# Optimization experiments

Measured on AMD Instinct MI355X. Metric: run time of the kernel, lower is better.

Reference implementation:

```python
import jax, jax.numpy as jnp
import numpy as np

T = 0.2


def _cdist(a, b):
    # Euclidean cdist with zero-safe sqrt (grad 0 at coincident points, like torch)
    d2 = (a * a).sum(-1)[:, None] + (b * b).sum(-1)[None, :] - 2.0 * (a @ b.T)
    d2 = jnp.maximum(d2, 0.0)
    safe = jnp.where(d2 > 0, d2, 1.0)
    return jnp.where(d2 > 0, jnp.sqrt(safe), 0.0)


def _generator(eps, W_in, b_in, W_blk, b_blk, W_out, b_out):
    x = eps @ W_in.T + b_in
    for i in range(W_blk.shape[0]):  # 4 residual MLP blocks
        x = x + jax.nn.relu(x @ W_blk[i].T + b_blk[i])
    return x @ W_out.T + b_out


def setup_inputs() -> dict:
    N, D, H = 4096, 128, 512
    key = jax.random.key(0)
    ks = jax.random.split(key, 16)

    def lin(kw, kb, fan_in, shape_w, shape_b):
        bound = 1.0 / np.sqrt(fan_in)
        W = jax.random.uniform(kw, shape_w, jnp.float32, -bound, bound)
        b = jax.random.uniform(kb, shape_b, jnp.float32, -bound, bound)
        return W, b

    W_in, b_in = lin(ks[0], ks[1], D, (H, D), (H,))
    W_blk, b_blk = lin(ks[2], ks[3], H, (4, H, H), (4, H))
    W_out, b_out = lin(ks[4], ks[5], H, (D, H), (D,))
    y_pos = jax.random.normal(ks[6], (N, D), jnp.float32)
    eps = jax.random.normal(ks[7], (N, D), jnp.float32)
    return {"y_pos": y_pos, "eps": eps, "W_in": W_in, "b_in": b_in,
            "W_blk": W_blk, "b_blk": b_blk, "W_out": W_out, "b_out": b_out}


def reference(y_pos, eps, W_in, b_in, W_blk, b_blk, W_out, b_out):
    x = _generator(eps, W_in, b_in, W_blk, b_blk, W_out, b_out)  # [N, D]
    N = y_pos.shape[0]
    dist_pos = _cdist(x, y_pos)                                   # [N, N]
    dist_neg = _cdist(x, x) + jnp.eye(x.shape[0], dtype=x.dtype) * 1e6
    A = jnp.concatenate([-dist_pos / T, -dist_neg / T], axis=-1)  # [N, 2N]
    A_row = jax.nn.softmax(A, axis=-1)
    A_col = jax.nn.softmax(A, axis=-2)
    A_soft = jnp.sqrt(A_row * A_col)
    A_pos = A_soft[:, :N]
    A_neg = A_soft[:, N:]
    s_pos = A_pos.sum(axis=1, keepdims=True)
    s_neg = A_neg.sum(axis=1, keepdims=True)
    Wpos = A_pos * s_neg
    # torch in-place: Wpos *= s_neg mutates A_pos BEFORE A_pos.sum is taken,
    # so Wneg = A_neg * (A_pos * s_neg).sum(1) = A_neg * s_pos * s_neg
    Wneg = A_neg * (s_pos * s_neg)
    V = Wpos @ y_pos - Wneg @ x                                   # drifting field
    target = jax.lax.stop_gradient(x + V)
    return jnp.mean((x - target) ** 2)
```

## Files before the change

kernel.cpp:

```cpp
#include <hip/hip_runtime.h>
#include <math.h>

#define N 4096
#define D 128
#define H 512
#define KSPLIT 4
#define SC_LOG2 7.2134752044f

typedef short bf16x8 __attribute__((ext_vector_type(8)));
typedef float f32x4 __attribute__((ext_vector_type(4)));
typedef unsigned short u16x8 __attribute__((ext_vector_type(8)));
typedef unsigned short u16;
typedef _Float16 f16;
typedef _Float16 f16x4 __attribute__((ext_vector_type(4)));

#define MFMA(a, b, c) __builtin_amdgcn_mfma_f32_16x16x32_bf16((a), (b), (c), 0, 0, 0)
#define SCHED_FENCE() __builtin_amdgcn_sched_barrier(0)

__device__ __forceinline__ float fexp2(float x)
{
#if __has_builtin(__builtin_amdgcn_exp2f)
    return __builtin_amdgcn_exp2f(x);
#else
    return exp2f(x);
#endif
}

__device__ __forceinline__ float fsqrt(float x)
{
#if __has_builtin(__builtin_amdgcn_sqrtf)
    return __builtin_amdgcn_sqrtf(x);
#else
    return sqrtf(x);
#endif
}

__device__ __forceinline__ float bf2f(u16 h)
{
    return __uint_as_float(((unsigned)h) << 16);
}

__device__ __forceinline__ u16 rtn_bf16(float v)
{
    unsigned u = __float_as_uint(v);
    return (u16)((u + 0x7FFFu + ((u >> 16) & 1u)) >> 16);
}

__device__ __forceinline__ void split1(float v, u16& h, u16& l)
{
    u16 hh = rtn_bf16(v);
    float r = v - bf2f(hh);
    h = hh;
    l = rtn_bf16(r);
}

__device__ __forceinline__ void split1_trunc(float v, u16& h, u16& l)
{
    unsigned bv = __float_as_uint(v);
    unsigned hb = bv & 0xFFFF0000u;
    float r = v - __uint_as_float(hb);
    h = (u16)(hb >> 16);
    l = (u16)(__float_as_uint(r) >> 16);
}

template <int CTRL>
__device__ __forceinline__ float dppf(float x)
{
    int r = __builtin_amdgcn_update_dpp(0, __float_as_int(x), CTRL, 0xF, 0xF, true);
    return __int_as_float(r);
}

struct SplitDesc { const float* src; u16* h; int n; };
struct SplitArgs { SplitDesc d[4]; };

__global__ __launch_bounds__(256) void split_multi(SplitArgs args)
{
    SplitDesc de = args.d[blockIdx.y];
    int idx = (blockIdx.x * 256 + threadIdx.x) * 4;
    if (idx >= de.n) return;
    float4 v = *(const float4*)(de.src + idx);
    ushort4 hv;
    hv.x = rtn_bf16(v.x); hv.y = rtn_bf16(v.y);
    hv.z = rtn_bf16(v.z); hv.w = rtn_bf16(v.w);
    *(ushort4*)(de.h + idx) = hv;
}

template <int K, bool RR>
__device__ __forceinline__ void gen_layer(
    u16 (&XhS)[16][520], u16 (&XlS)[16][520],
    const u16* __restrict__ W, const float* __restrict__ bias,
    int w, int quad, int l16)
{
    const int nb = w * 64;
    constexpr int NT = K >> 5;
    constexpr int PF = NT < 4 ? NT : 4;
    f32x4 acc[4] = {};
    const u16* wp[4];
    #pragma unroll
    for (int ni = 0; ni < 4; ++ni)
        wp[ni] = W + (size_t)(nb + ni * 16 + l16) * K + quad * 8;
    float bl4[4];
    #pragma unroll
    for (int ni = 0; ni < 4; ++ni) bl4[ni] = bias[nb + ni * 16 + l16];
    bf16x8 B[PF][4];
    #pragma unroll
    for (int s = 0; s < PF; ++s)
        #pragma unroll
        for (int ni = 0; ni < 4; ++ni)
            B[s][ni] = *(const bf16x8*)(wp[ni] + s * 32);
    SCHED_FENCE();
    #pragma unroll
    for (int kt = 0; kt < NT; ++kt) {
        const int kk = kt * 32 + quad * 8;
        bf16x8 af  = *(const bf16x8*)&XhS[l16][kk];
        bf16x8 alf = *(const bf16x8*)&XlS[l16][kk];
        #pragma unroll
        for (int ni = 0; ni < 4; ++ni) {
            acc[ni] = MFMA(af,  B[kt % PF][ni], acc[ni]);
            acc[ni] = MFMA(alf, B[kt % PF][ni], acc[ni]);
        }
        SCHED_FENCE();
        if (kt + PF < NT) {
            #pragma unroll
            for (int ni = 0; ni < 4; ++ni)
                B[kt % PF][ni] = *(const bf16x8*)(wp[ni] + (kt + PF) * 32);
        }
        SCHED_FENCE();
    }
    __syncthreads();
    #pragma unroll
    for (int ni = 0; ni < 4; ++ni) {
        const int col = nb + ni * 16 + l16;
        #pragma unroll
        for (int r = 0; r < 4; ++r) {
            const int row = quad * 4 + r;
            float v = acc[ni][r] + bl4[ni];
            if (RR) {
                float prev = bf2f(XhS[row][col]) + bf2f(XlS[row][col]);
                v = prev + fmaxf(v, 0.0f);
            }
            u16 hh, ll;
            split1_trunc(v, hh, ll);
            XhS[row][col] = hh;
            XlS[row][col] = ll;
        }
    }
    __syncthreads();
}

__global__ __launch_bounds__(512, 2) void gen_fused(
    const float* __restrict__ eps,
    const u16* __restrict__ Win, const u16* __restrict__ Wblk,
    const u16* __restrict__ Wout,
    const float* __restrict__ b_in, const float* __restrict__ b_blk,
    const float* __restrict__ b_out,
    float* __restrict__ xo, u16* __restrict__ xh)
{
    __shared__ u16 XhS[16][520], XlS[16][520];
    const int t = threadIdx.x;
    const int w = t >> 6, lane = t & 63;
    const int quad = lane >> 4, l16 = lane & 15;
    const int bm = blockIdx.x * 16;

    {
        int idx = t * 4;
        int row = idx >> 7, col = idx & 127;
        float4 v = *(const float4*)(eps + (size_t)(bm + row) * D + col);
        ushort4 hv, lv;
        split1(v.x, hv.x, lv.x); split1(v.y, hv.y, lv.y);
        split1(v.z, hv.z, lv.z); split1(v.w, hv.w, lv.w);
        *(ushort4*)&XhS[row][col] = hv;
        *(ushort4*)&XlS[row][col] = lv;
    }
    __syncthreads();

    gen_layer<D, false>(XhS, XlS, Win, b_in, w, quad, l16);
    for (int i = 0; i < 4; ++i)
        gen_layer<H, true>(XhS, XlS, Wblk + (size_t)i * H * H, b_blk + i * H,
                           w, quad, l16);

    {
        const int n0 = w * 16;
        constexpr int NT = H >> 5;
        constexpr int PF = 4;
        f32x4 acc5 = {};
        const u16* wp = Wout + (size_t)(n0 + l16) * H + quad * 8;
        const float bl = b_out[n0 + l16];
        bf16x8 B5[PF];
        #pragma unroll
        for (int s = 0; s < PF; ++s)
            B5[s] = *(const bf16x8*)(wp + s * 32);
        SCHED_FENCE();
        #pragma unroll
        for (int kt = 0; kt < NT; ++kt) {
            const int kk = kt * 32 + quad * 8;
            bf16x8 af  = *(const bf16x8*)&XhS[l16][kk];
            bf16x8 alf = *(const bf16x8*)&XlS[l16][kk];
            acc5 = MFMA(af,  B5[kt % PF], acc5);
            acc5 = MFMA(alf, B5[kt % PF], acc5);
            SCHED_FENCE();
            if (kt + PF < NT)
                B5[kt % PF] = *(const bf16x8*)(wp + (kt + PF) * 32);
            SCHED_FENCE();
        }
        const int col = n0 + l16;
        #pragma unroll
        for (int r = 0; r < 4; ++r) {
            const int gm = bm + quad * 4 + r;
            float v = acc5[r] + bl;
            xo[(size_t)gm * D + col] = v;
            xh[(size_t)gm * D + col] = rtn_bf16(v);
        }
    }
}

__global__ __launch_bounds__(256) void rownorm(
    const float* __restrict__ X, const float* __restrict__ Y,
    float* __restrict__ nx, float* __restrict__ ny)
{
    const float* src = blockIdx.y ? Y : X;
    float* dst = blockIdx.y ? ny : nx;
    const int t = threadIdx.x;
    const int row = blockIdx.x * 64 + (t >> 2);
    const int q = t & 3;
    const float* rp = src + (size_t)row * D + q * 32;
    float s = 0.f;
    #pragma unroll
    for (int i = 0; i < 8; ++i) {
        float4 v = *(const float4*)(rp + i * 4);
        s += v.x * v.x + v.y * v.y + v.z * v.z + v.w * v.w;
    }
    s += __shfl_xor(s, 1);
    s += __shfl_xor(s, 2);
    if (q == 0) dst[row] = s;
}

__global__ __launch_bounds__(256) void transpose_rtn(
    const float* __restrict__ X, const float* __restrict__ Y,
    u16* __restrict__ Xth, u16* __restrict__ Yth)
{
    const float* src = blockIdx.z ? Y : X;
    u16* th = blockIdx.z ? Yth : Xth;
    __shared__ float tile[32][33];
    const int t = threadIdx.x;
    const int r0 = blockIdx.x * 32, c0 = blockIdx.y * 32;
    {
        int rit = t >> 3, coff = (t & 7) * 4;
        float4 v = *(const float4*)(src + (size_t)(r0 + rit) * D + c0 + coff);
        tile[rit][coff + 0] = v.x; tile[rit][coff + 1] = v.y;
        tile[rit][coff + 2] = v.z; tile[rit][coff + 3] = v.w;
    }
    __syncthreads();
    {
        int cit = t >> 3, roff = (t & 7) * 4;
        ushort4 hv;
        hv.x = rtn_bf16(tile[roff + 0][cit]);
        hv.y = rtn_bf16(tile[roff + 1][cit]);
        hv.z = rtn_bf16(tile[roff + 2][cit]);
        hv.w = rtn_bf16(tile[roff + 3][cit]);
        *(ushort4*)(th + (size_t)(c0 + cit) * N + r0 + roff) = hv;
    }
}

__global__ __launch_bounds__(256) void dist_fused(
    const u16* __restrict__ Xh, const u16* __restrict__ Yh,
    const float* __restrict__ nx, const float* __restrict__ ny,
    f16* __restrict__ Apos, f16* __restrict__ Aneg,
    float* __restrict__ prm_p, float* __restrict__ prs_p,
    float* __restrict__ pcm_p, float* __restrict__ pcs_p,
    float* __restrict__ prm_n, float* __restrict__ prs_n)
{
    const int mat = blockIdx.z;
    const u16* Bhp = mat ? Xh : Yh;
    const float* nb = mat ? nx : ny;
    f16* Out = mat ? Aneg : Apos;
    float* prm = mat ? prm_n : prm_p;
    float* prs = mat ? prs_n : prs_p;

    __shared__ u16 XhS[128][40], YhS[128][40];
    const int t = threadIdx.x;
    const int w = t >> 6, lane = t & 63;
    const int quad = lane >> 4, l16 = lane & 15;
    const int bm = blockIdx.y * 128, bn = blockIdx.x * 128;
    f32x4 acc[2][8] = {};

    for (int k0 = 0; k0 < D; k0 += 32) {
        __syncthreads();
        #pragma unroll
        for (int p = 0; p < 2; ++p) {
            int slot = t + p * 256;
            int row = slot >> 2, koff = (slot & 3) << 3;
            *(u16x8*)&XhS[row][koff] =
                *(const u16x8*)(Xh + (size_t)(bm + row) * D + k0 + koff);
        }
        #pragma unroll
        for (int p = 0; p < 2; ++p) {
            int slot = t + p * 256;
            int row = slot >> 2, koff = (slot & 3) << 3;
            int pr = ((row & 3) << 4) | ((row & 63) >> 2) | (row & 64);
            int kf = koff ^ (((pr >> 4) & 3) << 3);
            *(u16x8*)&YhS[pr][kf] =
                *(const u16x8*)(Bhp + (size_t)(bn + row) * D + k0 + koff);
        }
        __syncthreads();
        bf16x8 af[2], bhf[8];
        #pragma unroll
        for (int mi = 0; mi < 2; ++mi)
            af[mi] = *(const bf16x8*)&XhS[w * 32 + mi * 16 + l16][quad * 8];
        #pragma unroll
        for (int ni = 0; ni < 8; ++ni) {
            int nn = ni & 3, hf = ni >> 2;
            bhf[ni] = *(const bf16x8*)
                &YhS[hf * 64 + nn * 16 + l16][(quad * 8) ^ (nn << 3)];
        }
        #pragma unroll
        for (int mi = 0; mi < 2; ++mi)
            #pragma unroll
            for (int ni = 0; ni < 8; ++ni)
                acc[mi][ni] = MFMA(af[mi], bhf[ni], acc[mi][ni]);
    }
    const int jb = bn + (l16 << 2);
    const float SC2 = SC_LOG2 * SC_LOG2;
    const float c2 = -2.0f * SC2;
    const float4 n0v = *(const float4*)(nb + jb);
    const float4 n1v = *(const float4*)(nb + jb + 64);
    const float nl[8] = {n0v.x * SC2, n0v.y * SC2, n0v.z * SC2, n0v.w * SC2,
                         n1v.x * SC2, n1v.y * SC2, n1v.z * SC2, n1v.w * SC2};
    #pragma unroll
    for (int mi = 0; mi < 2; ++mi)
        #pragma unroll
        for (int r = 0; r < 4; ++r) {
            const int gm = bm + w * 32 + mi * 16 + quad * 4 + r;
            const float nxm = nx[gm] * SC2;
            f16x4 ov0, ov1;
            #pragma unroll
            for (int nn = 0; nn < 4; ++nn) {
                float s0 = fsqrt(fmaxf(
                    fmaf(acc[mi][nn][r], c2, nxm + nl[nn]), 0.f));
                float s1 = fsqrt(fmaxf(
                    fmaf(acc[mi][4 + nn][r], c2, nxm + nl[4 + nn]), 0.f));
                if (mat) {
                    if (gm == jb + nn) s0 = 5.0e6f;
                    if (gm == jb + 64 + nn) s1 = 5.0e6f;
                }
                acc[mi][nn][r] = s0;
                acc[mi][4 + nn][r] = s1;
                ov0[nn] = (f16)(-s0);
                ov1[nn] = (f16)(-s1);
            }
            *(f16x4*)(Out + (size_t)gm * N + jb) = ov0;
            *(f16x4*)(Out + (size_t)gm * N + jb + 64) = ov1;
        }
    float m[2][4];
    #pragma unroll
    for (int mi = 0; mi < 2; ++mi)
        #pragma unroll
        for (int r = 0; r < 4; ++r) {
            float v = fminf(fminf(fminf(acc[mi][0][r], acc[mi][1][r]),
                                  fminf(acc[mi][2][r], acc[mi][3][r])),
                            fminf(fminf(acc[mi][4][r], acc[mi][5][r]),
                                  fminf(acc[mi][6][r], acc[mi][7][r])));
            v = fminf(v, dppf<0xB1>(v));
            v = fminf(v, dppf<0x4E>(v));
            v = fminf(v, dppf<0x141>(v));
            v = fminf(v, dppf<0x140>(v));
            m[mi][r] = v;
        }
    float mn = fminf(fminf(fminf(m[0][0], m[0][1]), fminf(m[0][2], m[0][3])),
                     fminf(fminf(m[1][0], m[1][1]), fminf(m[1][2], m[1][3])));
    mn = fminf(mn, __shfl_xor(mn, 16));
    mn = fminf(mn, __shfl_xor(mn, 32));
    float sig[2][4] = {};
    float cs[8] = {};
    #pragma unroll
    for (int mi = 0; mi < 2; ++mi)
        #pragma unroll
        for (int ni = 0; ni < 8; ++ni) {
            float e0 = fexp2(mn - acc[mi][ni][0]);
            float e1 = fexp2(mn - acc[mi][ni][1]);
            float e2 = fexp2(mn - acc[mi][ni][2]);
            float e3 = fexp2(mn - acc[mi][ni][3]);
            sig[mi][0] += e0; sig[mi][1] += e1;
            sig[mi][2] += e2; sig[mi][3] += e3;
            cs[ni] += (e0 + e1) + (e2 + e3);
        }
    const int ct = blockIdx.x;
    #pragma unroll
    for (int mi = 0; mi < 2; ++mi)
        #pragma unroll
        for (int r = 0; r < 4; ++r) {
            float s = sig[mi][r];
            s += dppf<0xB1>(s);
            s += dppf<0x4E>(s);
            s += dppf<0x141>(s);
            s += dppf<0x140>(s);
            s *= fexp2(m[mi][r] - mn);
            if (l16 == 0) {
                int grow = bm + w * 32 + mi * 16 + quad * 4 + r;
                prm[(size_t)ct * N + grow] = -m[mi][r];
                prs[(size_t)ct * N + grow] = s;
            }
        }
    if (mat == 0) {
        const int rt = blockIdx.y * 4 + w;
        #pragma unroll
        for (int ni = 0; ni < 8; ++ni) {
            cs[ni] += __shfl_xor(cs[ni], 16);
            cs[ni] += __shfl_xor(cs[ni], 32);
        }
        if (quad == 0) {
            float4 c0 = {cs[0], cs[1], cs[2], cs[3]};
            float4 c1 = {cs[4], cs[5], cs[6], cs[7]};
            float4 m4 = {-mn, -mn, -mn, -mn};
            *(float4*)(pcs_p + (size_t)rt * N + jb) = c0;
            *(float4*)(pcs_p + (size_t)rt * N + jb + 64) = c1;
            *(float4*)(pcm_p + (size_t)rt * N + jb) = m4;
            *(float4*)(pcm_p + (size_t)rt * N + jb + 64) = m4;
        }
    }
}

__global__ __launch_bounds__(256) void stats_combine(
    const float* __restrict__ prm_p, const float* __restrict__ prs_p,
    const float* __restrict__ prm_n, const float* __restrict__ prs_n,
    const float* __restrict__ pcm_p, const float* __restrict__ pcs_p,
    float* __restrict__ m_row, float* __restrict__ isr,
    float* __restrict__ m_col, float* __restrict__ isc)
{
    __shared__ float Ms[4][64], Ss[4][64];
    const int t = threadIdx.x;
    const int g = t >> 6, l = t & 63;
    const int idx = blockIdx.x * 64 + l;

    float m = -3.0e38f, s = 0.f;
    if (idx < N) {
        const int i = idx;
        const int c0 = g * 8;
        #pragma unroll 4
        for (int c = c0; c < c0 + 8; ++c) {
            m = fmaxf(m, prm_p[(size_t)c * N + i]);
            m = fmaxf(m, prm_n[(size_t)c * N + i]);
        }
        #pragma unroll 4
        for (int c = c0; c < c0 + 8; ++c) {
            s += prs_p[(size_t)c * N + i] * fexp2(prm_p[(size_t)c * N + i] - m);
            s += prs_n[(size_t)c * N + i] * fexp2(prm_n[(size_t)c * N + i] - m);
        }
    } else {
        const int mat = (idx - N) >> 12;
        const int j = idx & (N - 1);
        const float* pm = mat ? prm_n : pcm_p;
        const float* ps = mat ? prs_n : pcs_p;
        const int cnt = mat ? 8 : 32;
        const int cb = g * cnt;
        #pragma unroll 4
        for (int c = cb; c < cb + cnt; ++c)
            m = fmaxf(m, pm[(size_t)c * N + j]);
        #pragma unroll 4
        for (int c = cb; c < cb + cnt; ++c)
            s += ps[(size_t)c * N + j] * fexp2(pm[(size_t)c * N + j] - m);
    }
    Ms[g][l] = m; Ss[g][l] = s;
    __syncthreads();
    if (g == 0) {
        float m0 = Ms[0][l], m1 = Ms[1][l], m2 = Ms[2][l], m3 = Ms[3][l];
        float mm = fmaxf(fmaxf(m0, m1), fmaxf(m2, m3));
        float ss = Ss[0][l] * fexp2(m0 - mm) + Ss[1][l] * fexp2(m1 - mm)
                 + Ss[2][l] * fexp2(m2 - mm) + Ss[3][l] * fexp2(m3 - mm);
        if (idx < N) {
            m_row[idx] = mm;
            isr[idx] = 1.0f / sqrtf(ss);
        } else {
            const int mat = (idx - N) >> 12;
            const int j = idx & (N - 1);
            m_col[mat * N + j] = mm;
            isc[mat * N + j] = 1.0f / sqrtf(ss);
        }
    }
}

__global__ __launch_bounds__(256) void pv_mfma(
    const f16* __restrict__ Apos, const f16* __restrict__ Aneg,
    const u16* __restrict__ Yth, const u16* __restrict__ Xth,
    const float* __restrict__ m_row, const float* __restrict__ isr,
    const float* __restrict__ m_col, const float* __restrict__ isc,
    float* __restrict__ u_part, float* __restrict__ w_part,
    float* __restrict__ sp_part, float* __restrict__ sn_part)
{
    const int mat = blockIdx.z;
    const f16* Am = mat ? Aneg : Apos;
    const u16* Bh = mat ? Xth : Yth;
    const float* mc = m_col + mat * N;
    const float* ic = isc + mat * N;
    float* Cp = (mat ? w_part : u_part) + (size_t)blockIdx.y * (N * D);
    float* spn = (mat ? sn_part : sp_part) + (size_t)blockIdx.y * N;

    __shared__ u16 BhS[128][72];
    __shared__ u16 PhS[64][72], PlS[64][72];
    __shared__ float mrS[64], isrS[64];

    const int t = threadIdx.x;
    const int w = t >> 6, lane = t & 63;
    const int quad = lane >> 4, l16 = lane & 15;
    const int bm = blockIdx.x * 64;
    const int jbase = blockIdx.y * (N / KSPLIT);
    const int arow = t >> 4;
    const int aj = (t & 15) << 2;

    if (t < 64) { mrS[t] = m_row[bm + t]; isrS[t] = isr[bm + t]; }

    f32x4 acc[8] = {};
    float rs[4] = {0.f, 0.f, 0.f, 0.f};

    for (int jt = 0; jt < (N / KSPLIT) / 64; ++jt) {
        const int j0 = jbase + jt * 64;
        __syncthreads();
        #pragma unroll
        for (int p = 0; p < 4; ++p) {
            int slot = t + p * 256;
            int d = slot >> 3, joff = (slot & 7) << 3;
            *(u16x8*)&BhS[d][joff] = *(const u16x8*)(Bh + (size_t)d * N + j0 + joff);
        }
        float4 mcv = *(const float4*)(mc + j0 + aj);
        float4 icv = *(const float4*)(ic + j0 + aj);
        #pragma unroll
        for (int s = 0; s < 4; ++s) {
            int row = arow + s * 16;
            f16x4 av = *(const f16x4*)(Am + (size_t)(bm + row) * N + j0 + aj);
            float mr = mrS[row], sr = isrS[row];
            float p0 = fexp2((float)av.x - 0.5f * (mr + mcv.x)) * (sr * icv.x);
            float p1 = fexp2((float)av.y - 0.5f * (mr + mcv.y)) * (sr * icv.y);
            float p2 = fexp2((float)av.z - 0.5f * (mr + mcv.z)) * (sr * icv.z);
            float p3 = fexp2((float)av.w - 0.5f * (mr + mcv.w)) * (sr * icv.w);
            rs[s] += p0 + p1 + p2 + p3;
            ushort4 hv, lv;
            split1_trunc(p0, hv.x, lv.x); split1_trunc(p1, hv.y, lv.y);
            split1_trunc(p2, hv.z, lv.z); split1_trunc(p3, hv.w, lv.w);
            *(ushort4*)&PhS[row][aj] = hv;
            *(ushort4*)&PlS[row][aj] = lv;
        }
        __syncthreads();
        #pragma unroll
        for (int ks = 0; ks < 2; ++ks) {
            const int kk = ks * 32 + quad * 8;
            bf16x8 ph = *(const bf16x8*)&PhS[w * 16 + l16][kk];
            bf16x8 pl = *(const bf16x8*)&PlS[w * 16 + l16][kk];
            #pragma unroll
            for (int ni = 0; ni < 8; ++ni) {
                bf16x8 bh = *(const bf16x8*)&BhS[ni * 16 + l16][kk];
                acc[ni] = MFMA(ph, bh, acc[ni]);
                acc[ni] = MFMA(pl, bh, acc[ni]);
            }
        }
    }
    #pragma unroll
    for (int ni = 0; ni < 8; ++ni)
        #pragma unroll
        for (int r = 0; r < 4; ++r) {
            int row = w * 16 + quad * 4 + r;
            int col = ni * 16 + l16;
            Cp[(size_t)(bm + row) * D + col] = acc[ni][r];
        }
    #pragma unroll
    for (int s = 0; s < 4; ++s) {
        float v = rs[s];
        v += __shfl_xor(v, 1); v += __shfl_xor(v, 2);
        v += __shfl_xor(v, 4); v += __shfl_xor(v, 8);
        if (l16 == 0) spn[bm + arow + s * 16] = v;
    }
}

__global__ __launch_bounds__(256) void final_reduce(const float* __restrict__ u_part,
    const float* __restrict__ w_part, const float* __restrict__ sp_part,
    const float* __restrict__ sn_part, double* __restrict__ acc_part)
{
    __shared__ float red[256];
    const int t = threadIdx.x;
    const int idx = blockIdx.x * 256 + t;
    float u = 0.f, w = 0.f;
    #pragma unroll
    for (int c = 0; c < KSPLIT; ++c) {
        u += u_part[(size_t)c * (N * D) + idx];
        w += w_part[(size_t)c * (N * D) + idx];
    }
    const int i = idx >> 7;
    float sp = 0.f, sn = 0.f;
    #pragma unroll
    for (int c = 0; c < KSPLIT; ++c) {
        sp += sp_part[(size_t)c * N + i];
        sn += sn_part[(size_t)c * N + i];
    }
    const float v = sn * u - sp * sn * w;
    red[t] = v * v; __syncthreads();
    for (int s = 128; s > 0; s >>= 1) { if (t < s) red[t] += red[t + s]; __syncthreads(); }
    if (!t) acc_part[blockIdx.x] = (double)red[0];
}

__global__ __launch_bounds__(256) void finalize(const double* __restrict__ acc_part,
                                                float* __restrict__ out)
{
    __shared__ double red[256];
    const int t = threadIdx.x;
    double s = 0.0;
    #pragma unroll
    for (int i = 0; i < 8; ++i) s += acc_part[t + i * 256];
    red[t] = s; __syncthreads();
    for (int st = 128; st > 0; st >>= 1) {
        if (t < st) red[t] += red[t + st];
        __syncthreads();
    }
    if (!t) out[0] = (float)(red[0] * (1.0 / ((double)N * (double)D)));
}

extern "C" void kernel_launch(void* const* d_in, const int* in_sizes, int n_in,
                              void* d_out, int out_size, void* d_ws, size_t ws_size,
                              hipStream_t stream)
{
    const float* y_pos = (const float*)d_in[0];
    const float* eps   = (const float*)d_in[1];
    const float* W_in  = (const float*)d_in[2];
    const float* b_in  = (const float*)d_in[3];
    const float* W_blk = (const float*)d_in[4];
    const float* b_blk = (const float*)d_in[5];
    const float* W_out = (const float*)d_in[6];
    const float* b_out = (const float*)d_in[7];
    float* out = (float*)d_out;
    (void)in_sizes; (void)n_in; (void)out_size; (void)ws_size;

    char* p = (char*)d_ws;
    auto alloc = [&](size_t bytes) {
        char* r = p;
        p += (bytes + 255) & ~(size_t)255;
        return r;
    };
    double* acc_part = (double*)alloc(2048 * 8);
    float* sp_part = (float*)alloc((size_t)KSPLIT * N * 4);
    float* sn_part = (float*)alloc((size_t)KSPLIT * N * 4);
    float* m_row  = (float*)alloc(N * 4);
    float* isr    = (float*)alloc(N * 4);
    float* m_col  = (float*)alloc(2 * N * 4);
    float* isc    = (float*)alloc(2 * N * 4);
    float* nx     = (float*)alloc(N * 4);
    float* ny     = (float*)alloc(N * 4);
    float* xo  = (float*)alloc((size_t)N * D * 4);
    u16* xh    = (u16*)alloc((size_t)N * D * 2);
    u16* xth   = (u16*)alloc((size_t)N * D * 2);
    u16* yh    = (u16*)alloc((size_t)N * D * 2);
    u16* yth   = (u16*)alloc((size_t)N * D * 2);
    char* genreg = alloc((size_t)KSPLIT * N * D * 4 * 2);
    u16* wih = (u16*)genreg;
    u16* wbh = wih + (size_t)H * D;
    u16* woh = wbh + (size_t)4 * H * H;
    float* prm_p = (float*)genreg;
    float* prs_p = prm_p + 32 * N;
    float* prm_n = prs_p + 32 * N;
    float* prs_n = prm_n + 32 * N;
    float* pcm_p = prs_n + 32 * N;
    float* pcs_p = pcm_p + 128 * N;
    float* u_part = (float*)genreg;
    float* w_part = u_part + (size_t)KSPLIT * N * D;
    f16* Apos = (f16*)alloc((size_t)N * N * 2);
    f16* Aneg = (f16*)alloc((size_t)N * N * 2);

    SplitArgs sa;
    sa.d[0] = { y_pos, yh,  N * D };
    sa.d[1] = { W_in,  wih, H * D };
    sa.d[2] = { W_blk, wbh, 4 * H * H };
    sa.d[3] = { W_out, woh, D * H };
    split_multi<<<dim3(1024, 4), 256, 0, stream>>>(sa);

    gen_fused<<<N / 16, 512, 0, stream>>>(eps, wih, wbh, woh,
                                          b_in, b_blk, b_out, xo, xh);

    rownorm<<<dim3(N / 64, 2), 256, 0, stream>>>(xo, y_pos, nx, ny);

    transpose_rtn<<<dim3(N / 32, D / 32, 2), 256, 0, stream>>>(
        xo, y_pos, xth, yth);

    dist_fused<<<dim3(N / 128, N / 128, 2), 256, 0, stream>>>(
        xh, yh, nx, ny, Apos, Aneg,
        prm_p, prs_p, pcm_p, pcs_p, prm_n, prs_n);

    stats_combine<<<192, 256, 0, stream>>>(prm_p, prs_p, prm_n, prs_n,
                                           pcm_p, pcs_p,
                                           m_row, isr, m_col, isc);

    pv_mfma<<<dim3(N / 64, KSPLIT, 2), 256, 0, stream>>>(Apos, Aneg,
        yth, xth, m_row, isr, m_col, isc, u_part, w_part, sp_part, sn_part);

    final_reduce<<<(N * D) / 256, 256, 0, stream>>>(u_part, w_part,
                                                    sp_part, sn_part, acc_part);
    finalize<<<1, 256, 0, stream>>>(acc_part, out);
}
```

Baseline: 230.3 us.

## Pre-pack generator weights into MFMA fragment layout and use 1024-thread blocks

The weight conversion kernel now writes generator weights in a packed layout ordered by k-tile, quad and output column, so each lane's bf16x8 fragment load is contiguous across the wavefront and coalesced. The fused generator kernel moves to 1024 threads with 16 waves, each owning 32 output columns instead of 64. The explicit register prefetch pipeline and scheduling fences are dropped in favour of a simple two-k-tile unrolled loop. This halves per-wave accumulators and register pressure and improves weight-load coalescing, but it relies on the compiler to hide global load latency and leaves half the waves idle in the output layer.

```diff
diff --git a/kernel.cpp b/kernel.cpp
--- a/kernel.cpp
+++ b/kernel.cpp
@@ -15,7 +15,6 @@
 typedef _Float16 f16x4 __attribute__((ext_vector_type(4)));
 
 #define MFMA(a, b, c) __builtin_amdgcn_mfma_f32_16x16x32_bf16((a), (b), (c), 0, 0, 0)
-#define SCHED_FENCE() __builtin_amdgcn_sched_barrier(0)
 
 __device__ __forceinline__ float fexp2(float x)
 {
@@ -70,7 +69,7 @@
     return __int_as_float(r);
 }
 
-struct SplitDesc { const float* src; u16* h; int n; };
+struct SplitDesc { const float* src; u16* h; int n; int ks; int os; };
 struct SplitArgs { SplitDesc d[4]; };
 
 __global__ __launch_bounds__(256) void split_multi(SplitArgs args)
@@ -82,59 +81,63 @@
     ushort4 hv;
     hv.x = rtn_bf16(v.x); hv.y = rtn_bf16(v.y);
     hv.z = rtn_bf16(v.z); hv.w = rtn_bf16(v.w);
-    *(ushort4*)(de.h + idx) = hv;
+    if (de.ks < 0) {
+        *(ushort4*)(de.h + idx) = hv;
+    } else {
+        const int ks = de.ks, os = de.os;
+        const int lsz = 1 << (ks + os);
+        const int layer = idx >> (ks + os);
+        const int fl = idx & (lsz - 1);
+        const int col = fl >> ks;
+        const int k = fl & ((1 << ks) - 1);
+        const int kt = k >> 5, quad = (k >> 3) & 3, j = k & 7;
+        const int pidx = layer * lsz + (((((kt << 2) + quad) << os) + col) << 3) + j;
+        *(ushort4*)(de.h + pidx) = hv;
+    }
 }
 
 template <int K, bool RR>
 __device__ __forceinline__ void gen_layer(
     u16 (&XhS)[16][520], u16 (&XlS)[16][520],
-    const u16* __restrict__ W, const float* __restrict__ bias,
+    const u16* __restrict__ Wp, const float* __restrict__ bias,
     int w, int quad, int l16)
 {
-    const int nb = w * 64;
+    const int nb = w * 32;
     constexpr int NT = K >> 5;
-    constexpr int PF = NT < 4 ? NT : 4;
-    f32x4 acc[4] = {};
-    const u16* wp[4];
-    #pragma unroll
-    for (int ni = 0; ni < 4; ++ni)
-        wp[ni] = W + (size_t)(nb + ni * 16 + l16) * K + quad * 8;
-    float bl4[4];
-    #pragma unroll
-    for (int ni = 0; ni < 4; ++ni) bl4[ni] = bias[nb + ni * 16 + l16];
-    bf16x8 B[PF][4];
-    #pragma unroll
-    for (int s = 0; s < PF; ++s)
-        #pragma unroll
-        for (int ni = 0; ni < 4; ++ni)
-            B[s][ni] = *(const bf16x8*)(wp[ni] + s * 32);
-    SCHED_FENCE();
-    #pragma unroll
-    for (int kt = 0; kt < NT; ++kt) {
-        const int kk = kt * 32 + quad * 8;
-        bf16x8 af  = *(const bf16x8*)&XhS[l16][kk];
-        bf16x8 alf = *(const bf16x8*)&XlS[l16][kk];
-        #pragma unroll
-        for (int ni = 0; ni < 4; ++ni) {
-            acc[ni] = MFMA(af,  B[kt % PF][ni], acc[ni]);
-            acc[ni] = MFMA(alf, B[kt % PF][ni], acc[ni]);
-        }
-        SCHED_FENCE();
-        if (kt + PF < NT) {
-            #pragma unroll
-            for (int ni = 0; ni < 4; ++ni)
-                B[kt % PF][ni] = *(const bf16x8*)(wp[ni] + (kt + PF) * 32);
-        }
-        SCHED_FENCE();
+    f32x4 acc[2] = {};
+    float bl2[2];
+    bl2[0] = bias[nb + l16];
+    bl2[1] = bias[nb + 16 + l16];
+    const u16* wb = Wp + (size_t)quad * 4096 + (size_t)nb * 8 + (size_t)l16 * 8;
+    #pragma unroll
+    for (int kc = 0; kc < NT / 2; ++kc) {
+        const int kta = 2 * kc, ktb = 2 * kc + 1;
+        bf16x8 b0[2], b1[2];
+        b0[0] = *(const bf16x8*)(wb + kta * 16384);
+        b0[1] = *(const bf16x8*)(wb + kta * 16384 + 128);
+        b1[0] = *(const bf16x8*)(wb + ktb * 16384);
+        b1[1] = *(const bf16x8*)(wb + ktb * 16384 + 128);
+        bf16x8 a0h = *(const bf16x8*)&XhS[l16][kta * 32 + quad * 8];
+        bf16x8 a0l = *(const bf16x8*)&XlS[l16][kta * 32 + quad * 8];
+        bf16x8 a1h = *(const bf16x8*)&XhS[l16][ktb * 32 + quad * 8];
+        bf16x8 a1l = *(const bf16x8*)&XlS[l16][ktb * 32 + quad * 8];
+        acc[0] = MFMA(a0h, b0[0], acc[0]);
+        acc[0] = MFMA(a0l, b0[0], acc[0]);
+        acc[1] = MFMA(a0h, b0[1], acc[1]);
+        acc[1] = MFMA(a0l, b0[1], acc[1]);
+        acc[0] = MFMA(a1h, b1[0], acc[0]);
+        acc[0] = MFMA(a1l, b1[0], acc[0]);
+        acc[1] = MFMA(a1h, b1[1], acc[1]);
+        acc[1] = MFMA(a1l, b1[1], acc[1]);
     }
     __syncthreads();
     #pragma unroll
-    for (int ni = 0; ni < 4; ++ni) {
+    for (int ni = 0; ni < 2; ++ni) {
         const int col = nb + ni * 16 + l16;
         #pragma unroll
         for (int r = 0; r < 4; ++r) {
             const int row = quad * 4 + r;
-            float v = acc[ni][r] + bl4[ni];
+            float v = acc[ni][r] + bl2[ni];
             if (RR) {
                 float prev = bf2f(XhS[row][col]) + bf2f(XlS[row][col]);
                 v = prev + fmaxf(v, 0.0f);
@@ -148,7 +151,7 @@
     __syncthreads();
 }
 
-__global__ __launch_bounds__(512, 2) void gen_fused(
+__global__ __launch_bounds__(1024) void gen_fused(
     const float* __restrict__ eps,
     const u16* __restrict__ Win, const u16* __restrict__ Wblk,
     const u16* __restrict__ Wout,
@@ -163,45 +166,42 @@
     const int bm = blockIdx.x * 16;
 
     {
-        int idx = t * 4;
+        int idx = t * 2;
         int row = idx >> 7, col = idx & 127;
-        float4 v = *(const float4*)(eps + (size_t)(bm + row) * D + col);
-        ushort4 hv, lv;
+        float2 v = *(const float2*)(eps + (size_t)(bm + row) * D + col);
+        ushort2 hv, lv;
         split1(v.x, hv.x, lv.x); split1(v.y, hv.y, lv.y);
-        split1(v.z, hv.z, lv.z); split1(v.w, hv.w, lv.w);
-        *(ushort4*)&XhS[row][col] = hv;
-        *(ushort4*)&XlS[row][col] = lv;
+        *(ushort2*)&XhS[row][col] = hv;
+        *(ushort2*)&XlS[row][col] = lv;
     }
     __syncthreads();
 
     gen_layer<D, false>(XhS, XlS, Win, b_in, w, quad, l16);
+    #pragma unroll 1
     for (int i = 0; i < 4; ++i)
         gen_layer<H, true>(XhS, XlS, Wblk + (size_t)i * H * H, b_blk + i * H,
                            w, quad, l16);
 
-    {
+    if (w < 8) {
         const int n0 = w * 16;
         constexpr int NT = H >> 5;
-        constexpr int PF = 4;
         f32x4 acc5 = {};
-        const u16* wp = Wout + (size_t)(n0 + l16) * H + quad * 8;
         const float bl = b_out[n0 + l16];
-        bf16x8 B5[PF];
-        #pragma unroll
-        for (int s = 0; s < PF; ++s)
-            B5[s] = *(const bf16x8*)(wp + s * 32);
-        SCHED_FENCE();
-        #pragma unroll
-        for (int kt = 0; kt < NT; ++kt) {
-            const int kk = kt * 32 + quad * 8;
-            bf16x8 af  = *(const bf16x8*)&XhS[l16][kk];
-            bf16x8 alf = *(const bf16x8*)&XlS[l16][kk];
-            acc5 = MFMA(af,  B5[kt % PF], acc5);
-            acc5 = MFMA(alf, B5[kt % PF], acc5);
-            SCHED_FENCE();
-            if (kt + PF < NT)
-                B5[kt % PF] = *(const bf16x8*)(wp + (kt + PF) * 32);
-            SCHED_FENCE();
+        const u16* wb = Wout + (size_t)quad * 1024 + (size_t)n0 * 8
+                             + (size_t)l16 * 8;
+        #pragma unroll
+        for (int kc = 0; kc < NT / 2; ++kc) {
+            const int kta = 2 * kc, ktb = 2 * kc + 1;
+            bf16x8 b0 = *(const bf16x8*)(wb + kta * 4096);
+            bf16x8 b1 = *(const bf16x8*)(wb + ktb * 4096);
+            bf16x8 a0h = *(const bf16x8*)&XhS[l16][kta * 32 + quad * 8];
+            bf16x8 a0l = *(const bf16x8*)&XlS[l16][kta * 32 + quad * 8];
+            bf16x8 a1h = *(const bf16x8*)&XhS[l16][ktb * 32 + quad * 8];
+            bf16x8 a1l = *(const bf16x8*)&XlS[l16][ktb * 32 + quad * 8];
+            acc5 = MFMA(a0h, b0, acc5);
+            acc5 = MFMA(a0l, b0, acc5);
+            acc5 = MFMA(a1h, b1, acc5);
+            acc5 = MFMA(a1l, b1, acc5);
         }
         const int col = n0 + l16;
         #pragma unroll
@@ -663,14 +663,14 @@
     f16* Aneg = (f16*)alloc((size_t)N * N * 2);
 
     SplitArgs sa;
-    sa.d[0] = { y_pos, yh,  N * D };
-    sa.d[1] = { W_in,  wih, H * D };
-    sa.d[2] = { W_blk, wbh, 4 * H * H };
-    sa.d[3] = { W_out, woh, D * H };
+    sa.d[0] = { y_pos, yh,  N * D,     -1, 0 };
+    sa.d[1] = { W_in,  wih, H * D,      7, 9 };
+    sa.d[2] = { W_blk, wbh, 4 * H * H,  9, 9 };
+    sa.d[3] = { W_out, woh, D * H,      9, 7 };
     split_multi<<<dim3(1024, 4), 256, 0, stream>>>(sa);
 
-    gen_fused<<<N / 16, 512, 0, stream>>>(eps, wih, wbh, woh,
-                                          b_in, b_blk, b_out, xo, xh);
+    gen_fused<<<N / 16, 1024, 0, stream>>>(eps, wih, wbh, woh,
+                                           b_in, b_blk, b_out, xo, xh);
 
     rownorm<<<dim3(N / 64, 2), 256, 0, stream>>>(xo, y_pos, nx, ny);
 
```

After: 191.4 us, median of 2. 16.9% less time.
